# Optimization experiments

Measured on AMD Instinct MI355X. Metric: run time of the kernel, lower is better.

Reference implementation:

```python
import jax, jax.numpy as jnp
import numpy as np

B, S, D, E, H, F, L, C = 32768, 5, 512, 256, 4, 2048, 2, 5  # batch, sensors, input_dim, embed_dim, heads, ffn, layers, classes
DH = E // H
EPS = 1e-5


def layer_norm(x, g, b):
    m = jnp.mean(x, axis=-1, keepdims=True)
    v = jnp.mean((x - m) ** 2, axis=-1, keepdims=True)
    return (x - m) * jax.lax.rsqrt(v + EPS) * g + b


def setup_inputs() -> dict:
    key = jax.random.key(0)
    ks = jax.random.split(key, 24)
    n = lambda k, shape: (jax.random.normal(k, shape, dtype=jnp.float32) * 0.02)
    return {
        "x": jax.random.normal(ks[0], (B, S, D), dtype=jnp.float32),
        "sensor_types": jax.random.randint(ks[1], (B, S), 0, 2, dtype=jnp.int32),
        "gps_w": n(ks[2], (E, D)), "gps_b": jnp.zeros((E,), jnp.float32),
        "ang_w": n(ks[3], (E, D)), "ang_b": jnp.zeros((E,), jnp.float32),
        "qkv_w": n(ks[4], (L, 3 * E, E)), "qkv_b": jnp.zeros((L, 3 * E), jnp.float32),
        "attn_ow": n(ks[5], (L, E, E)), "attn_ob": jnp.zeros((L, E), jnp.float32),
        "ln1_g": jnp.ones((L, E), jnp.float32), "ln1_b": jnp.zeros((L, E), jnp.float32),
        "ff1_w": n(ks[6], (L, F, E)), "ff1_b": jnp.zeros((L, F), jnp.float32),
        "ff2_w": n(ks[7], (L, E, F)), "ff2_b": jnp.zeros((L, E), jnp.float32),
        "ln2_g": jnp.ones((L, E), jnp.float32), "ln2_b": jnp.zeros((L, E), jnp.float32),
        "fc1_w": n(ks[8], (128, S * E)), "fc1_b": jnp.zeros((128,), jnp.float32),
        "fc2_w": n(ks[9], (64, 128)), "fc2_b": jnp.zeros((64,), jnp.float32),
        "out_w": n(ks[10], (C, 64)), "out_b": jnp.zeros((C,), jnp.float32),
    }


def reference(x, sensor_types, gps_w, gps_b, ang_w, ang_b, qkv_w, qkv_b,
              attn_ow, attn_ob, ln1_g, ln1_b, ff1_w, ff1_b, ff2_w, ff2_b,
              ln2_g, ln2_b, fc1_w, fc1_b, fc2_w, fc2_b, out_w, out_b):
    # Dual-expert routing: compute both branches, blend by mask (same math as masked scatter)
    is_gps = (sensor_types == 0)[..., None]  # [B,S,1]
    g = jax.nn.relu(jnp.einsum('bsd,ed->bse', x, gps_w) + gps_b)
    a = jax.nn.relu(jnp.einsum('bsd,ed->bse', x, ang_w) + ang_b)
    h = jnp.where(is_gps, g, a)  # [B,S,E]

    # TransformerEncoder (post-LN, ReLU FFN, dropout inactive at eval)
    for l in range(L):
        qkv = jnp.einsum('bse,fe->bsf', h, qkv_w[l]) + qkv_b[l]  # [B,S,3E]
        q, k, v = jnp.split(qkv, 3, axis=-1)
        q = q.reshape(B, S, H, DH); k = k.reshape(B, S, H, DH); v = v.reshape(B, S, H, DH)
        scores = jnp.einsum('bqhd,bkhd->bhqk', q, k) / jnp.sqrt(jnp.float32(DH))
        attn = jax.nn.softmax(scores, axis=-1)
        o = jnp.einsum('bhqk,bkhd->bqhd', attn, v).reshape(B, S, E)
        o = o @ attn_ow[l].T + attn_ob[l]
        h = layer_norm(h + o, ln1_g[l], ln1_b[l])
        ff = jax.nn.relu(h @ ff1_w[l].T + ff1_b[l]) @ ff2_w[l].T + ff2_b[l]
        h = layer_norm(h + ff, ln2_g[l], ln2_b[l])

    z = h.reshape(B, S * E)
    z = z @ fc1_w.T + fc1_b
    z = z @ fc2_w.T + fc2_b
    return z @ out_w.T + out_b
```

## Files before the change

kernel.cpp:

```cpp
#include <hip/hip_runtime.h>


#define N_TOK 163840
#define NBATCH 32768

typedef __attribute__((ext_vector_type(8))) short bfrag;
typedef __attribute__((ext_vector_type(4))) float f32x4;

__device__ __forceinline__ float bf2f(ushort u) {
  return __builtin_bit_cast(float, (uint)u << 16);
}
__device__ __forceinline__ ushort f2bf(float f) {
  uint u = __builtin_bit_cast(uint, f);
  return (ushort)((u + 0x7FFFu + ((u >> 16) & 1u)) >> 16);
}

__global__ __launch_bounds__(256) void cvt_kernel(const float* __restrict__ in,
                                                  ushort* __restrict__ out, int n4) {
  int i = blockIdx.x * 256 + threadIdx.x;
  if (i >= n4) return;
  float4 v = ((const float4*)in)[i];
  ushort4 o;
  o.x = f2bf(v.x); o.y = f2bf(v.y); o.z = f2bf(v.z); o.w = f2bf(v.w);
  ((ushort4*)out)[i] = o;
}

enum { EPI_F32 = 0, EPI_F32_RELU = 1, EPI_BF16 = 2, EPI_BF16_RELU = 3, EPI_SELECT = 4 };

template <int EPI>
__global__ __launch_bounds__(256) void gemm_bt(const ushort* __restrict__ A,
                                               const ushort* __restrict__ W,
                                               const float* __restrict__ bias,
                                               void* __restrict__ outp,
                                               int M, int K, int O,
                                               const float* __restrict__ gbuf,
                                               const int* __restrict__ stype,
                                               ushort* __restrict__ h16out) {
  __shared__ ushort As[128][40];
  __shared__ ushort Bs[128][40];
  const int tid = threadIdx.x;
  const int wave = tid >> 6, lane = tid & 63;
  const int bm = blockIdx.y, bn = blockIdx.x;
  const int wm = (wave & 1) << 6, wn = (wave >> 1) << 6;
  const int srow = tid >> 2;
  const int scol = (tid & 3) << 3;

  const ushort* Abase = A + (size_t)(bm * 128 + srow) * K + scol;
  const ushort* Wbase = W + (size_t)(bn * 128 + srow) * K + scol;

  f32x4 acc[4][4];
#pragma unroll
  for (int i = 0; i < 4; i++)
#pragma unroll
    for (int j = 0; j < 4; j++) acc[i][j] = {0.f, 0.f, 0.f, 0.f};

  const int fr = lane & 15;
  const int fkb = (lane >> 4) << 3;

  uint4 a0 = *(const uint4*)(Abase);
  uint4 a1 = *(const uint4*)(Abase + (size_t)64 * K);
  uint4 b0 = *(const uint4*)(Wbase);
  uint4 b1 = *(const uint4*)(Wbase + (size_t)64 * K);

  for (int k0 = 0; k0 < K; k0 += 32) {
    *(uint4*)&As[srow][scol]      = a0;
    *(uint4*)&As[srow + 64][scol] = a1;
    *(uint4*)&Bs[srow][scol]      = b0;
    *(uint4*)&Bs[srow + 64][scol] = b1;
    __syncthreads();
    if (k0 + 32 < K) {
      a0 = *(const uint4*)(Abase + k0 + 32);
      a1 = *(const uint4*)(Abase + k0 + 32 + (size_t)64 * K);
      b0 = *(const uint4*)(Wbase + k0 + 32);
      b1 = *(const uint4*)(Wbase + k0 + 32 + (size_t)64 * K);
    }
    bfrag af[4], bf_[4];
#pragma unroll
    for (int i = 0; i < 4; i++) af[i] = *(const bfrag*)&As[wm + i * 16 + fr][fkb];
#pragma unroll
    for (int j = 0; j < 4; j++) bf_[j] = *(const bfrag*)&Bs[wn + j * 16 + fr][fkb];
#pragma unroll
    for (int i = 0; i < 4; i++)
#pragma unroll
      for (int j = 0; j < 4; j++)
        acc[i][j] = __builtin_amdgcn_mfma_f32_16x16x32_bf16(af[i], bf_[j], acc[i][j], 0, 0, 0);
    __syncthreads();
  }

  const int cr = (lane >> 4) << 2;
  const int cc = lane & 15;
#pragma unroll
  for (int j = 0; j < 4; j++) {
    const int col = bn * 128 + wn + j * 16 + cc;
    const float bv = bias[col];
#pragma unroll
    for (int i = 0; i < 4; i++) {
      const int row = bm * 128 + wm + i * 16 + cr;
#pragma unroll
      for (int r = 0; r < 4; r++) {
        float v = acc[i][j][r] + bv;
        const size_t idx = (size_t)(row + r) * O + col;
        if (EPI != EPI_F32 && EPI != EPI_BF16) v = fmaxf(v, 0.f);
        if (EPI == EPI_SELECT) {
          if (stype[row + r] == 0) v = gbuf[idx];
          ((float*)outp)[idx] = v;
          h16out[idx] = f2bf(v);
        } else if (EPI == EPI_F32 || EPI == EPI_F32_RELU) {
          ((float*)outp)[idx] = v;
        } else {
          ((ushort*)outp)[idx] = f2bf(v);
        }
      }
    }
  }
}

__global__ __launch_bounds__(512) void gemm_lnres(const ushort* __restrict__ A,
                                                  const ushort* __restrict__ W,
                                                  const float* __restrict__ bias,
                                                  float* __restrict__ h32,
                                                  ushort* __restrict__ h16,
                                                  const float* __restrict__ g,
                                                  const float* __restrict__ b,
                                                  int K) {
  __shared__ ushort As[128][40];
  __shared__ ushort Bs[256][40];
  __shared__ float2 s_part[128][4];
  __shared__ float2 s_mr[128];
  const int tid = threadIdx.x;
  const int wave = tid >> 6, lane = tid & 63;
  const int bm = blockIdx.x;
  const int wm = (wave & 1) << 6, wn = (wave >> 1) << 6;

  const int srow = tid >> 2;
  const int scol = (tid & 3) << 3;
  const ushort* Ag = A + (size_t)(bm * 128 + srow) * K + scol;
  const ushort* Wg = W + (size_t)srow * K + scol;

  f32x4 acc[4][4];
#pragma unroll
  for (int i = 0; i < 4; i++)
#pragma unroll
    for (int j = 0; j < 4; j++) acc[i][j] = {0.f, 0.f, 0.f, 0.f};

  const int fr = lane & 15;
  const int fkb = (lane >> 4) << 3;

  uint4 a0 = *(const uint4*)(Ag);
  uint4 b0 = *(const uint4*)(Wg);
  uint4 b1 = *(const uint4*)(Wg + (size_t)128 * K);

  for (int k0 = 0; k0 < K; k0 += 32) {
    *(uint4*)&As[srow][scol]       = a0;
    *(uint4*)&Bs[srow][scol]       = b0;
    *(uint4*)&Bs[srow + 128][scol] = b1;
    __syncthreads();
    if (k0 + 32 < K) {
      a0 = *(const uint4*)(Ag + k0 + 32);
      b0 = *(const uint4*)(Wg + k0 + 32);
      b1 = *(const uint4*)(Wg + k0 + 32 + (size_t)128 * K);
    }
    bfrag af[4], bf_[4];
#pragma unroll
    for (int i = 0; i < 4; i++) af[i] = *(const bfrag*)&As[wm + i * 16 + fr][fkb];
#pragma unroll
    for (int j = 0; j < 4; j++) bf_[j] = *(const bfrag*)&Bs[wn + j * 16 + fr][fkb];
#pragma unroll
    for (int i = 0; i < 4; i++)
#pragma unroll
      for (int j = 0; j < 4; j++)
        acc[i][j] = __builtin_amdgcn_mfma_f32_16x16x32_bf16(af[i], bf_[j], acc[i][j], 0, 0, 0);
    __syncthreads();
  }

  const int cr = (lane >> 4) << 2;
  const int cc = lane & 15;
#pragma unroll
  for (int i = 0; i < 4; i++) {
#pragma unroll
    for (int r = 0; r < 4; r++) {
      const int row = wm + i * 16 + cr + r;
      const size_t grow = (size_t)(bm * 128 + row) * 256;
      float s = 0.f, sq = 0.f;
#pragma unroll
      for (int j = 0; j < 4; j++) {
        const int col = wn + j * 16 + cc;
        float u = acc[i][j][r] + bias[col] + h32[grow + col];
        acc[i][j][r] = u;
        s += u; sq += u * u;
      }
#pragma unroll
      for (int o = 1; o < 16; o <<= 1) { s += __shfl_xor(s, o); sq += __shfl_xor(sq, o); }
      if ((lane & 15) == 0) s_part[row][wave >> 1] = {s, sq};
    }
  }
  __syncthreads();
  if (tid < 128) {
    float2 p0 = s_part[tid][0], p1 = s_part[tid][1], p2 = s_part[tid][2], p3 = s_part[tid][3];
    float S = p0.x + p1.x + p2.x + p3.x;
    float SQ = p0.y + p1.y + p2.y + p3.y;
    float mean = S * 0.00390625f;
    float var = SQ * 0.00390625f - mean * mean;
    s_mr[tid] = {mean, rsqrtf(var + 1e-5f)};
  }
  __syncthreads();
#pragma unroll
  for (int i = 0; i < 4; i++) {
#pragma unroll
    for (int r = 0; r < 4; r++) {
      const int row = wm + i * 16 + cr + r;
      const float2 mr = s_mr[row];
      const size_t grow = (size_t)(bm * 128 + row) * 256;
#pragma unroll
      for (int j = 0; j < 4; j++) {
        const int col = wn + j * 16 + cc;
        float y = (acc[i][j][r] - mr.x) * mr.y * g[col] + b[col];
        h32[grow + col] = y;
        h16[grow + col] = f2bf(y);
      }
    }
  }
}

__global__ __launch_bounds__(256) void attn_kernel(const ushort* __restrict__ qkv,
                                                   ushort* __restrict__ o16) {
  __shared__ ushort s_qkv[8 * 5 * 768];
  __shared__ float s_att[8 * 4 * 25];
  const int tid = threadIdx.x;
  const size_t gbase = (size_t)blockIdx.x * (8 * 5 * 768);
#pragma unroll
  for (int t = 0; t < 15; t++) {
    int i = tid + t * 256;
    *(uint4*)&s_qkv[i * 8] = *(const uint4*)(qkv + gbase + (size_t)i * 8);
  }
  __syncthreads();
  for (int idx = tid; idx < 800; idx += 256) {
    int b = idx / 100, r = idx - b * 100;
    int h = r / 25, ij = r - h * 25;
    int i = ij / 5, j = ij - i * 5;
    const ushort* qp = &s_qkv[(b * 5 + i) * 768 + h * 64];
    const ushort* kp = &s_qkv[(b * 5 + j) * 768 + 256 + h * 64];
    float s = 0.f;
#pragma unroll
    for (int d = 0; d < 64; d += 2) {
      uint qw = *(const uint*)&qp[d];
      uint kw = *(const uint*)&kp[d];
      s += bf2f((ushort)(qw & 0xffffu)) * bf2f((ushort)(kw & 0xffffu));
      s += bf2f((ushort)(qw >> 16)) * bf2f((ushort)(kw >> 16));
    }
    s_att[idx] = s * 0.125f;
  }
  __syncthreads();
  if (tid < 160) {
    float* sp = &s_att[tid * 5];
    float m = fmaxf(fmaxf(fmaxf(sp[0], sp[1]), fmaxf(sp[2], sp[3])), sp[4]);
    float e0 = __expf(sp[0] - m), e1 = __expf(sp[1] - m), e2 = __expf(sp[2] - m);
    float e3 = __expf(sp[3] - m), e4 = __expf(sp[4] - m);
    float inv = 1.f / (e0 + e1 + e2 + e3 + e4);
    sp[0] = e0 * inv; sp[1] = e1 * inv; sp[2] = e2 * inv; sp[3] = e3 * inv; sp[4] = e4 * inv;
  }
  __syncthreads();
  const size_t obase = (size_t)blockIdx.x * (8 * 5 * 256);
#pragma unroll
  for (int t = 0; t < 40; t++) {
    int idx = t * 256 + tid;
    int d = idx & 63;
    int rest = idx >> 6;
    int h = rest & 3; rest >>= 2;
    int i = rest % 5, b = rest / 5;
    const float* ap = &s_att[(b * 4 + h) * 25 + i * 5];
    const ushort* vp = &s_qkv[(b * 5) * 768 + 512 + h * 64 + d];
    float o = 0.f;
#pragma unroll
    for (int j = 0; j < 5; j++) o += ap[j] * bf2f(vp[j * 768]);
    o16[obase + (size_t)((b * 5 + i) * 256 + h * 64 + d)] = f2bf(o);
  }
}

__global__ __launch_bounds__(256) void head2_kernel(const float* __restrict__ z1,
                                                    const float* __restrict__ fc2w,
                                                    const float* __restrict__ fc2b,
                                                    const float* __restrict__ outw,
                                                    const float* __restrict__ outb,
                                                    float* __restrict__ out) {
  __shared__ float s_z2[4][64];
  const int wave = threadIdx.x >> 6, lane = threadIdx.x & 63;
  const int b = blockIdx.x * 4 + wave;
  const float* z = z1 + (size_t)b * 128;
  float acc = fc2b[lane];
#pragma unroll 8
  for (int k = 0; k < 128; k++) acc += z[k] * fc2w[lane * 128 + k];
  s_z2[wave][lane] = acc;
  __syncthreads();
  if (lane < 5) {
    const float* zz = s_z2[wave];
    float o = outb[lane];
#pragma unroll 8
    for (int k = 0; k < 64; k++) o += zz[k] * outw[lane * 64 + k];
    out[(size_t)b * 5 + lane] = o;
  }
}

extern "C" void kernel_launch(void* const* d_in, const int* in_sizes, int n_in,
                              void* d_out, int out_size, void* d_ws, size_t ws_size,
                              hipStream_t stream) {
  const float* x       = (const float*)d_in[0];
  const int*   stype   = (const int*)d_in[1];
  const float* gps_w   = (const float*)d_in[2];
  const float* gps_b   = (const float*)d_in[3];
  const float* ang_w   = (const float*)d_in[4];
  const float* ang_b   = (const float*)d_in[5];
  const float* qkv_w   = (const float*)d_in[6];
  const float* qkv_b   = (const float*)d_in[7];
  const float* attn_ow = (const float*)d_in[8];
  const float* attn_ob = (const float*)d_in[9];
  const float* ln1_g   = (const float*)d_in[10];
  const float* ln1_b   = (const float*)d_in[11];
  const float* ff1_w   = (const float*)d_in[12];
  const float* ff1_b   = (const float*)d_in[13];
  const float* ff2_w   = (const float*)d_in[14];
  const float* ff2_b   = (const float*)d_in[15];
  const float* ln2_g   = (const float*)d_in[16];
  const float* ln2_b   = (const float*)d_in[17];
  const float* fc1_w   = (const float*)d_in[18];
  const float* fc1_b   = (const float*)d_in[19];
  const float* fc2_w   = (const float*)d_in[20];
  const float* fc2_b   = (const float*)d_in[21];
  const float* out_w   = (const float*)d_in[22];
  const float* out_b   = (const float*)d_in[23];

  char* ws = (char*)d_ws;
  const size_t NEED = 763363328ull;
  if (ws_size < NEED) return;

  ushort* w_gps  = (ushort*)ws;
  ushort* w_ang  = w_gps + 131072;
  ushort* w_qkv  = w_ang + 131072;
  ushort* w_attn = w_qkv + 393216;
  ushort* w_ff1  = w_attn + 131072;
  ushort* w_ff2  = w_ff1 + 1048576;
  ushort* w_fc1  = w_ff2 + 1048576;

  ushort* R16 = (ushort*)(ws + (size_t)(8u << 20));
  ushort* h16 = (ushort*)(ws + 8388608ull + 251658240ull);
  float*  h32 = (float*)(ws + 8388608ull + 251658240ull + 83886080ull);
  float*  t32 = (float*)(ws + 8388608ull + 251658240ull + 83886080ull + 167772160ull);
  ushort* o16 = (ushort*)(ws + 8388608ull + 251658240ull + 83886080ull + 335544320ull);

  auto cvt = [&](const float* src, ushort* dst, int n4) {
    cvt_kernel<<<(n4 + 255) / 256, 256, 0, stream>>>(src, dst, n4);
  };
  cvt(gps_w, w_gps, 32768);
  cvt(ang_w, w_ang, 32768);
  cvt(qkv_w, w_qkv, 98304);
  cvt(attn_ow, w_attn, 32768);
  cvt(ff1_w, w_ff1, 262144);
  cvt(ff2_w, w_ff2, 262144);
  cvt(fc1_w, w_fc1, 40960);
  cvt(x, R16, 20971520);

  gemm_bt<EPI_F32_RELU><<<dim3(2, 1280), 256, 0, stream>>>(
      R16, w_gps, gps_b, t32, N_TOK, 512, 256, nullptr, nullptr, nullptr);
  gemm_bt<EPI_SELECT><<<dim3(2, 1280), 256, 0, stream>>>(
      R16, w_ang, ang_b, h32, N_TOK, 512, 256, t32, stype, h16);

  for (int l = 0; l < 2; l++) {
    gemm_bt<EPI_BF16><<<dim3(6, 1280), 256, 0, stream>>>(
        h16, w_qkv + l * 196608, qkv_b + l * 768, R16, N_TOK, 256, 768,
        nullptr, nullptr, nullptr);
    attn_kernel<<<4096, 256, 0, stream>>>(R16, o16);
    gemm_lnres<<<1280, 512, 0, stream>>>(o16, w_attn + l * 65536, attn_ob + l * 256,
                                         h32, h16, ln1_g + l * 256, ln1_b + l * 256, 256);
    for (int c = 0; c < 4; c++) {
      gemm_bt<EPI_BF16_RELU><<<dim3(16, 320), 256, 0, stream>>>(
          h16 + (size_t)c * 40960 * 256, w_ff1 + l * 524288, ff1_b + l * 2048,
          R16, 40960, 256, 2048, nullptr, nullptr, nullptr);
      gemm_lnres<<<320, 512, 0, stream>>>(R16, w_ff2 + l * 524288, ff2_b + l * 256,
                                          h32 + (size_t)c * 40960 * 256,
                                          h16 + (size_t)c * 40960 * 256,
                                          ln2_g + l * 256, ln2_b + l * 256, 2048);
    }
  }

  gemm_bt<EPI_F32><<<dim3(1, 256), 256, 0, stream>>>(
      h16, w_fc1, fc1_b, t32, NBATCH, 1280, 128, nullptr, nullptr, nullptr);
  head2_kernel<<<8192, 256, 0, stream>>>(t32, fc2_w, fc2_b, out_w, out_b, (float*)d_out);
}
```

Baseline: 3.708 ms.

## Fuse FFN into single kernel keeping hidden activations on-chip; XOR-swizzle LDS tiles

```diff
diff --git a/kernel.cpp b/kernel.cpp
--- a/kernel.cpp
+++ b/kernel.cpp
@@ -36,14 +36,16 @@
                                                const float* __restrict__ gbuf,
                                                const int* __restrict__ stype,
                                                ushort* __restrict__ h16out) {
-  __shared__ ushort As[128][40];
-  __shared__ ushort Bs[128][40];
+  __shared__ ushort As[128][32];
+  __shared__ ushort Bs[128][32];
   const int tid = threadIdx.x;
   const int wave = tid >> 6, lane = tid & 63;
   const int bm = blockIdx.y, bn = blockIdx.x;
   const int wm = (wave & 1) << 6, wn = (wave >> 1) << 6;
   const int srow = tid >> 2;
-  const int scol = (tid & 3) << 3;
+  const int sq   = tid & 3;
+  const int sc   = ((sq ^ ((srow >> 2) & 3))) << 3;
+  const int scol = sq << 3;
 
   const ushort* Abase = A + (size_t)(bm * 128 + srow) * K + scol;
   const ushort* Wbase = W + (size_t)(bn * 128 + srow) * K + scol;
@@ -55,7 +57,8 @@
     for (int j = 0; j < 4; j++) acc[i][j] = {0.f, 0.f, 0.f, 0.f};
 
   const int fr = lane & 15;
-  const int fkb = (lane >> 4) << 3;
+  const int fq = lane >> 4;
+  const int rc = (fq ^ ((fr >> 2) & 3)) << 3;
 
   uint4 a0 = *(const uint4*)(Abase);
   uint4 a1 = *(const uint4*)(Abase + (size_t)64 * K);
@@ -63,10 +66,10 @@
   uint4 b1 = *(const uint4*)(Wbase + (size_t)64 * K);
 
   for (int k0 = 0; k0 < K; k0 += 32) {
-    *(uint4*)&As[srow][scol]      = a0;
-    *(uint4*)&As[srow + 64][scol] = a1;
-    *(uint4*)&Bs[srow][scol]      = b0;
-    *(uint4*)&Bs[srow + 64][scol] = b1;
+    *(uint4*)&As[srow][sc]      = a0;
+    *(uint4*)&As[srow + 64][sc] = a1;
+    *(uint4*)&Bs[srow][sc]      = b0;
+    *(uint4*)&Bs[srow + 64][sc] = b1;
     __syncthreads();
     if (k0 + 32 < K) {
       a0 = *(const uint4*)(Abase + k0 + 32);
@@ -76,9 +79,9 @@
     }
     bfrag af[4], bf_[4];
 #pragma unroll
-    for (int i = 0; i < 4; i++) af[i] = *(const bfrag*)&As[wm + i * 16 + fr][fkb];
-#pragma unroll
-    for (int j = 0; j < 4; j++) bf_[j] = *(const bfrag*)&Bs[wn + j * 16 + fr][fkb];
+    for (int i = 0; i < 4; i++) af[i] = *(const bfrag*)&As[wm + i * 16 + fr][rc];
+#pragma unroll
+    for (int j = 0; j < 4; j++) bf_[j] = *(const bfrag*)&Bs[wn + j * 16 + fr][rc];
 #pragma unroll
     for (int i = 0; i < 4; i++)
 #pragma unroll
@@ -87,8 +90,8 @@
     __syncthreads();
   }
 
-  const int cr = (lane >> 4) << 2;
-  const int cc = lane & 15;
+  const int cr = fq << 2;
+  const int cc = fr;
 #pragma unroll
   for (int j = 0; j < 4; j++) {
     const int col = bn * 128 + wn + j * 16 + cc;
@@ -123,8 +126,8 @@
                                                   const float* __restrict__ g,
                                                   const float* __restrict__ b,
                                                   int K) {
-  __shared__ ushort As[128][40];
-  __shared__ ushort Bs[256][40];
+  __shared__ ushort As[128][32];
+  __shared__ ushort Bs[256][32];
   __shared__ float2 s_part[128][4];
   __shared__ float2 s_mr[128];
   const int tid = threadIdx.x;
@@ -133,7 +136,9 @@
   const int wm = (wave & 1) << 6, wn = (wave >> 1) << 6;
 
   const int srow = tid >> 2;
-  const int scol = (tid & 3) << 3;
+  const int sq   = tid & 3;
+  const int sc   = ((sq ^ ((srow >> 2) & 3))) << 3;
+  const int scol = sq << 3;
   const ushort* Ag = A + (size_t)(bm * 128 + srow) * K + scol;
   const ushort* Wg = W + (size_t)srow * K + scol;
 
@@ -144,16 +149,17 @@
     for (int j = 0; j < 4; j++) acc[i][j] = {0.f, 0.f, 0.f, 0.f};
 
   const int fr = lane & 15;
-  const int fkb = (lane >> 4) << 3;
+  const int fq = lane >> 4;
+  const int rc = (fq ^ ((fr >> 2) & 3)) << 3;
 
   uint4 a0 = *(const uint4*)(Ag);
   uint4 b0 = *(const uint4*)(Wg);
   uint4 b1 = *(const uint4*)(Wg + (size_t)128 * K);
 
   for (int k0 = 0; k0 < K; k0 += 32) {
-    *(uint4*)&As[srow][scol]       = a0;
-    *(uint4*)&Bs[srow][scol]       = b0;
-    *(uint4*)&Bs[srow + 128][scol] = b1;
+    *(uint4*)&As[srow][sc]       = a0;
+    *(uint4*)&Bs[srow][sc]       = b0;
+    *(uint4*)&Bs[srow + 128][sc] = b1;
     __syncthreads();
     if (k0 + 32 < K) {
       a0 = *(const uint4*)(Ag + k0 + 32);
@@ -162,9 +168,9 @@
     }
     bfrag af[4], bf_[4];
 #pragma unroll
-    for (int i = 0; i < 4; i++) af[i] = *(const bfrag*)&As[wm + i * 16 + fr][fkb];
-#pragma unroll
-    for (int j = 0; j < 4; j++) bf_[j] = *(const bfrag*)&Bs[wn + j * 16 + fr][fkb];
+    for (int i = 0; i < 4; i++) af[i] = *(const bfrag*)&As[wm + i * 16 + fr][rc];
+#pragma unroll
+    for (int j = 0; j < 4; j++) bf_[j] = *(const bfrag*)&Bs[wn + j * 16 + fr][rc];
 #pragma unroll
     for (int i = 0; i < 4; i++)
 #pragma unroll
@@ -173,25 +179,25 @@
     __syncthreads();
   }
 
-  const int cr = (lane >> 4) << 2;
-  const int cc = lane & 15;
+  const int cr = fq << 2;
+  const int cc = fr;
 #pragma unroll
   for (int i = 0; i < 4; i++) {
 #pragma unroll
     for (int r = 0; r < 4; r++) {
       const int row = wm + i * 16 + cr + r;
       const size_t grow = (size_t)(bm * 128 + row) * 256;
-      float s = 0.f, sq = 0.f;
+      float s = 0.f, sq2 = 0.f;
 #pragma unroll
       for (int j = 0; j < 4; j++) {
         const int col = wn + j * 16 + cc;
         float u = acc[i][j][r] + bias[col] + h32[grow + col];
         acc[i][j][r] = u;
-        s += u; sq += u * u;
+        s += u; sq2 += u * u;
       }
 #pragma unroll
-      for (int o = 1; o < 16; o <<= 1) { s += __shfl_xor(s, o); sq += __shfl_xor(sq, o); }
-      if ((lane & 15) == 0) s_part[row][wave >> 1] = {s, sq};
+      for (int o = 1; o < 16; o <<= 1) { s += __shfl_xor(s, o); sq2 += __shfl_xor(sq2, o); }
+      if ((lane & 15) == 0) s_part[row][wave >> 1] = {s, sq2};
     }
   }
   __syncthreads();
@@ -217,6 +223,145 @@
         float y = (acc[i][j][r] - mr.x) * mr.y * g[col] + b[col];
         h32[grow + col] = y;
         h16[grow + col] = f2bf(y);
+      }
+    }
+  }
+}
+
+__global__ __launch_bounds__(512) void ffn_fused(const ushort* __restrict__ h16in,
+                                                 const ushort* __restrict__ W1,
+                                                 const float* __restrict__ b1,
+                                                 const ushort* __restrict__ W2,
+                                                 const float* __restrict__ b2,
+                                                 float* __restrict__ h32,
+                                                 ushort* __restrict__ h16out,
+                                                 const float* __restrict__ g,
+                                                 const float* __restrict__ bb) {
+  __shared__ ushort sh[128][264];
+  __shared__ ushort smid[128][136];
+  __shared__ float2 s_part[128][4];
+  __shared__ float2 s_mr[128];
+  const int tid = threadIdx.x;
+  const int wave = tid >> 6, lane = tid & 63;
+  const size_t tok0 = (size_t)blockIdx.x * 128;
+
+  {
+    const int r = tid >> 2, c0 = (tid & 3) << 6;
+    const ushort* src = h16in + (tok0 + r) * 256 + c0;
+#pragma unroll
+    for (int u = 0; u < 8; u++)
+      *(uint4*)&sh[r][c0 + u * 8] = *(const uint4*)(src + u * 8);
+  }
+
+  const int fr = lane & 15;
+  const int fq = lane >> 4;
+  const int cr = fq << 2;
+  const int cc = fr;
+  const int tm = (wave & 1) << 6;
+  const int mq = (wave >> 1) << 5;
+  const int oq = (wave >> 1) << 6;
+
+  f32x4 acc2[4][4];
+#pragma unroll
+  for (int i = 0; i < 4; i++)
+#pragma unroll
+    for (int j = 0; j < 4; j++) acc2[i][j] = {0.f, 0.f, 0.f, 0.f};
+
+  __syncthreads();
+
+  for (int c = 0; c < 16; c++) {
+    f32x4 acc1[4][2];
+#pragma unroll
+    for (int i = 0; i < 4; i++)
+#pragma unroll
+      for (int j = 0; j < 2; j++) acc1[i][j] = {0.f, 0.f, 0.f, 0.f};
+#pragma unroll 2
+    for (int k = 0; k < 8; k++) {
+      const int ko = k * 32 + fq * 8;
+      bfrag af[4], bf_[2];
+#pragma unroll
+      for (int i = 0; i < 4; i++) af[i] = *(const bfrag*)&sh[tm + i * 16 + fr][ko];
+#pragma unroll
+      for (int j = 0; j < 2; j++)
+        bf_[j] = *(const bfrag*)(W1 + (size_t)(c * 128 + mq + j * 16 + fr) * 256 + ko);
+#pragma unroll
+      for (int i = 0; i < 4; i++)
+#pragma unroll
+        for (int j = 0; j < 2; j++)
+          acc1[i][j] = __builtin_amdgcn_mfma_f32_16x16x32_bf16(af[i], bf_[j], acc1[i][j], 0, 0, 0);
+    }
+    __syncthreads();
+#pragma unroll
+    for (int j = 0; j < 2; j++) {
+      const float bv = b1[c * 128 + mq + j * 16 + cc];
+#pragma unroll
+      for (int i = 0; i < 4; i++)
+#pragma unroll
+        for (int r = 0; r < 4; r++) {
+          float v = fmaxf(acc1[i][j][r] + bv, 0.f);
+          smid[tm + i * 16 + cr + r][mq + j * 16 + cc] = f2bf(v);
+        }
+    }
+    __syncthreads();
+#pragma unroll 2
+    for (int k = 0; k < 4; k++) {
+      const int ko = k * 32 + fq * 8;
+      bfrag af[4], bf_[4];
+#pragma unroll
+      for (int i = 0; i < 4; i++) af[i] = *(const bfrag*)&smid[tm + i * 16 + fr][ko];
+#pragma unroll
+      for (int j = 0; j < 4; j++)
+        bf_[j] = *(const bfrag*)(W2 + (size_t)(oq + j * 16 + fr) * 2048 + c * 128 + ko);
+#pragma unroll
+      for (int i = 0; i < 4; i++)
+#pragma unroll
+        for (int j = 0; j < 4; j++)
+          acc2[i][j] = __builtin_amdgcn_mfma_f32_16x16x32_bf16(af[i], bf_[j], acc2[i][j], 0, 0, 0);
+    }
+  }
+
+#pragma unroll
+  for (int i = 0; i < 4; i++) {
+#pragma unroll
+    for (int r = 0; r < 4; r++) {
+      const int row = tm + i * 16 + cr + r;
+      const size_t grow = (tok0 + row) * 256;
+      float s = 0.f, sq2 = 0.f;
+#pragma unroll
+      for (int j = 0; j < 4; j++) {
+        const int col = oq + j * 16 + cc;
+        float u = acc2[i][j][r] + b2[col] + h32[grow + col];
+        acc2[i][j][r] = u;
+        s += u; sq2 += u * u;
+      }
+#pragma unroll
+      for (int o = 1; o < 16; o <<= 1) { s += __shfl_xor(s, o); sq2 += __shfl_xor(sq2, o); }
+      if ((lane & 15) == 0) s_part[row][wave >> 1] = {s, sq2};
+    }
+  }
+  __syncthreads();
+  if (tid < 128) {
+    float2 p0 = s_part[tid][0], p1 = s_part[tid][1], p2 = s_part[tid][2], p3 = s_part[tid][3];
+    float S = p0.x + p1.x + p2.x + p3.x;
+    float SQ = p0.y + p1.y + p2.y + p3.y;
+    float mean = S * 0.00390625f;
+    float var = SQ * 0.00390625f - mean * mean;
+    s_mr[tid] = {mean, rsqrtf(var + 1e-5f)};
+  }
+  __syncthreads();
+#pragma unroll
+  for (int i = 0; i < 4; i++) {
+#pragma unroll
+    for (int r = 0; r < 4; r++) {
+      const int row = tm + i * 16 + cr + r;
+      const float2 mr = s_mr[row];
+      const size_t grow = (tok0 + row) * 256;
+#pragma unroll
+      for (int j = 0; j < 4; j++) {
+        const int col = oq + j * 16 + cc;
+        float y = (acc2[i][j][r] - mr.x) * mr.y * g[col] + bb[col];
+        h32[grow + col] = y;
+        h16out[grow + col] = f2bf(y);
       }
     }
   }
@@ -371,15 +516,9 @@
     attn_kernel<<<4096, 256, 0, stream>>>(R16, o16);
     gemm_lnres<<<1280, 512, 0, stream>>>(o16, w_attn + l * 65536, attn_ob + l * 256,
                                          h32, h16, ln1_g + l * 256, ln1_b + l * 256, 256);
-    for (int c = 0; c < 4; c++) {
-      gemm_bt<EPI_BF16_RELU><<<dim3(16, 320), 256, 0, stream>>>(
-          h16 + (size_t)c * 40960 * 256, w_ff1 + l * 524288, ff1_b + l * 2048,
-          R16, 40960, 256, 2048, nullptr, nullptr, nullptr);
-      gemm_lnres<<<320, 512, 0, stream>>>(R16, w_ff2 + l * 524288, ff2_b + l * 256,
-                                          h32 + (size_t)c * 40960 * 256,
-                                          h16 + (size_t)c * 40960 * 256,
-                                          ln2_g + l * 256, ln2_b + l * 256, 2048);
-    }
+    ffn_fused<<<1280, 512, 0, stream>>>(h16, w_ff1 + l * 524288, ff1_b + l * 2048,
+                                        w_ff2 + l * 524288, ff2_b + l * 256,
+                                        h32, h16, ln2_g + l * 256, ln2_b + l * 256);
   }
 
   gemm_bt<EPI_F32><<<dim3(1, 256), 256, 0, stream>>>(
```

Result: faster. 3.389 ms (-8.6%).
